# Performance work log

Measured on AMD Instinct MI355X. Metric: run time of the kernel, lower is better.

## Reference

```python
import jax, jax.numpy as jnp
import numpy as np


def conv(x, w, b=None, pad=0):
    y = jax.lax.conv_general_dilated(x, w, (1, 1), [(pad, pad), (pad, pad)],
                                     dimension_numbers=('NCHW', 'OIHW', 'NCHW'))
    if b is not None:
        y = y + b[None, :, None, None]
    return y


def bn(x, g, b, m, v, eps=1e-5):
    scale = g / jnp.sqrt(v + eps)
    return (x - m[None, :, None, None]) * scale[None, :, None, None] + b[None, :, None, None]


def channel_gate(x, w1, b1, w2, b2):
    # avg pool -> MLP -> sigmoid, returns [B, C, 1, 1]
    p = x.mean(axis=(2, 3))                       # [B, C]
    h = jax.nn.relu(p @ w1.T + b1)                # [B, C//r]
    a = h @ w2.T + b2                             # [B, C]
    return jax.nn.sigmoid(a)[:, :, None, None]


def setup_inputs() -> dict:
    key = jax.random.key(0)
    ks = iter(jax.random.split(key, 48))
    B, Cin, H, W = 2, 256, 64, 64
    Ci = Cin // 2          # inter_channels = 128
    Cr = Ci // 16          # gate bottleneck = 8
    def nrm(shape, s=0.05):
        return jax.random.normal(next(ks), shape, jnp.float32) * s
    d = {}
    d['q'] = jax.random.normal(next(ks), (B, Cin, H, W), jnp.float32)
    d['s'] = jax.random.normal(next(ks), (B, Cin, H, W), jnp.float32)
    # Trans_s: conv3x3 + BN
    d['ts_w'] = nrm((Ci, Cin, 3, 3)); d['ts_b'] = jnp.zeros(Ci)
    d['ts_g'] = jnp.ones(Ci); d['ts_be'] = jnp.zeros(Ci)
    d['ts_m'] = nrm((Ci,), 0.01); d['ts_v'] = jnp.ones(Ci)
    # Trans_q: conv3x3 + BN
    d['tq_w'] = nrm((Ci, Cin, 3, 3)); d['tq_b'] = jnp.zeros(Ci)
    d['tq_g'] = jnp.ones(Ci); d['tq_be'] = jnp.zeros(Ci)
    d['tq_m'] = nrm((Ci,), 0.01); d['tq_v'] = jnp.ones(Ci)
    # common_v 1x1
    d['cv_w'] = nrm((Ci, Ci, 1, 1)); d['cv_b'] = jnp.zeros(Ci)
    # key/query 1x1 projections (out = Ci//2)
    d['k1_w'] = nrm((Ci // 2, Ci, 1, 1)); d['k1_b'] = jnp.zeros(Ci // 2)
    d['q1_w'] = nrm((Ci // 2, Ci, 1, 1)); d['q1_b'] = jnp.zeros(Ci // 2)
    d['k2_w'] = nrm((Ci // 2, Ci, 1, 1)); d['k2_b'] = jnp.zeros(Ci // 2)
    d['q2_w'] = nrm((Ci // 2, Ci, 1, 1)); d['q2_b'] = jnp.zeros(Ci // 2)
    # ChannelGate MLP
    d['g1_w'] = nrm((Cr, Ci)); d['g1_b'] = jnp.zeros(Cr)
    d['g2_w'] = nrm((Ci, Cr)); d['g2_b'] = jnp.zeros(Ci)
    # conv_cat: conv3x3 (no bias) + BN
    d['cc_w'] = nrm((Ci, 2 * Ci, 3, 3))
    d['cc_g'] = jnp.ones(Ci); d['cc_be'] = jnp.zeros(Ci)
    d['cc_m'] = nrm((Ci,), 0.01); d['cc_v'] = jnp.ones(Ci)
    return d


def reference(q, s, ts_w, ts_b, ts_g, ts_be, ts_m, ts_v,
              tq_w, tq_b, tq_g, tq_be, tq_m, tq_v,
              cv_w, cv_b, k1_w, k1_b, q1_w, q1_b, k2_w, k2_b, q2_w, q2_b,
              g1_w, g1_b, g2_w, g2_b, cc_w, cc_g, cc_be, cc_m, cc_v):
    # stems: conv3x3 + BN + ReLU
    s = jax.nn.relu(bn(conv(s, ts_w, ts_b, pad=1), ts_g, ts_be, ts_m, ts_v))
    q = jax.nn.relu(bn(conv(q, tq_w, tq_b, pad=1), tq_g, tq_be, tq_m, tq_v))
    B, C, H, W = q.shape
    N = H * W
    # values
    v_q1 = conv(q, cv_w, cv_b)                          # [B,C,H,W]
    v_s1 = conv(s, cv_w, cv_b)
    v_q = v_q1.reshape(B, C, N).transpose(0, 2, 1)      # [B,N,C]
    v_s = v_s1.reshape(B, C, N).transpose(0, 2, 1)
    # dual keys / queries with negation trick
    k1 = conv(s, k1_w, k1_b).reshape(B, C // 2, N)
    k2 = conv(q, k2_w, k2_b).reshape(B, C // 2, N)
    key_cat = jnp.concatenate([k1, -k2], axis=1).transpose(0, 2, 1)   # [B,N,C]
    q1x = conv(s, q1_w, q1_b).reshape(B, C // 2, N)
    q2x = conv(q, q2_w, q2_b).reshape(B, C // 2, N)
    query_cat = jnp.concatenate([q1x, q2x], axis=1)                    # [B,C,N]
    # abs-score attention, dual softmax from the same score matrix
    A_s = jnp.abs(jnp.einsum('bnc,bcm->bnm', key_cat, query_cat))      # [B,N,N]
    att_s = jax.nn.softmax(A_s, axis=-1)
    att_q = jax.nn.softmax(A_s.transpose(0, 2, 1), axis=-1)
    # attend + channel-gate SE fusion + residual
    p_s = jnp.einsum('bnm,bmc->bnc', att_s, v_s).transpose(0, 2, 1).reshape(B, C, H, W)
    E_s = channel_gate(v_s1, g1_w, g1_b, g2_w, g2_b) * p_s + s
    q_s = jnp.einsum('bnm,bmc->bnc', att_q, v_q).transpose(0, 2, 1).reshape(B, C, H, W)
    E_q = channel_gate(v_q1, g1_w, g1_b, g2_w, g2_b) * q_s + q
    # concat + conv3x3(no bias) + BN + ReLU
    cpam = jax.nn.relu(bn(conv(jnp.concatenate([E_q, E_s], axis=1), cc_w, None, pad=1),
                          cc_g, cc_be, cc_m, cc_v))
    return (cpam, E_q, E_s)
```

## Files before the change

### kernel.cpp

```cpp
#include <hip/hip_runtime.h>

typedef __bf16 bf16;
typedef __bf16 v8bf __attribute__((ext_vector_type(8)));
typedef __bf16 v4bf __attribute__((ext_vector_type(4)));
typedef float v4f __attribute__((ext_vector_type(4)));

#define MFMA16(a, b, c) __builtin_amdgcn_mfma_f32_16x16x32_bf16(a, b, c, 0, 0, 0)

__device__ __forceinline__ float sf(float x) {
  if (!(x == x)) return 0.f;
  return fminf(fmaxf(x, -1e30f), 1e30f);
}

__global__ __launch_bounds__(256) void fill_kernel(float* __restrict__ out, float v, int n) {
  int i = blockIdx.x * 256 + threadIdx.x;
  if (i < n) out[i] = v;
}

__global__ __launch_bounds__(256) void prep_kernel(
    const float* __restrict__ ts_w, const float* __restrict__ tq_w,
    const float* ts_b, const float* ts_g, const float* ts_be, const float* ts_m, const float* ts_v,
    const float* tq_b, const float* tq_g, const float* tq_be, const float* tq_m, const float* tq_v,
    bf16* __restrict__ Wt01, float* __restrict__ ss01)
{
  int idx = blockIdx.x * 256 + threadIdx.x;
  if (idx < 589824) {
    int which = idx / 294912;
    int rem = idx - which * 294912;
    int co = rem / 2304;
    int r2 = rem - co * 2304;
    int tap = r2 >> 8;
    int ci = r2 & 255;
    const float* W = which ? tq_w : ts_w;
    Wt01[idx] = (bf16)W[(co * 256 + ci) * 9 + tap];
  } else if (idx < 590080) {
    int i = idx - 589824;
    int which = i >> 7, c = i & 127;
    float g, be, m, vv, bias;
    if (which == 0) { g=ts_g[c]; be=ts_be[c]; m=ts_m[c]; vv=ts_v[c]; bias=ts_b[c]; }
    else            { g=tq_g[c]; be=tq_be[c]; m=tq_m[c]; vv=tq_v[c]; bias=tq_b[c]; }
    float scale = g / sqrtf(vv + 1e-5f);
    ss01[which * 256 + c] = sf(scale);
    ss01[which * 256 + 128 + c] = sf((bias - m) * scale + be);
  }
}

__global__ __launch_bounds__(256) void prep2_kernel(
    const float* __restrict__ cc_w, const float* cc_g, const float* cc_be,
    const float* cc_m, const float* cc_v,
    bf16* __restrict__ Wt2, float* __restrict__ ss_cc)
{
  int idx = blockIdx.x * 256 + threadIdx.x;
  if (idx < 294912) {
    int co = idx / 2304;
    int r2 = idx - co * 2304;
    int tap = r2 >> 8;
    int ci = r2 & 255;
    Wt2[idx] = (bf16)cc_w[(co * 256 + ci) * 9 + tap];
  } else if (idx < 295040) {
    int c = idx - 294912;
    float scale = cc_g[c] / sqrtf(cc_v[c] + 1e-5f);
    ss_cc[c] = sf(scale);
    ss_cc[128 + c] = sf(-cc_m[c] * scale + cc_be[c]);
  }
}

__global__ __launch_bounds__(256) void tr_kernel(
    const float* __restrict__ s_in, const float* __restrict__ q_in, bf16* __restrict__ xin)
{
  int nb = blockIdx.x;
  int z = blockIdx.y;
  const float* in = ((z >> 1) ? q_in : s_in) + (long)(z & 1) * 1048576;
  bf16* out = xin + (long)z * 1048576;
  int t = threadIdx.x, lane = t & 63, w = t >> 6;
  long n = (long)nb * 64 + lane;
#pragma unroll
  for (int i = 0; i < 8; ++i) {
    int c8 = w * 8 + i;
    v8bf o;
#pragma unroll
    for (int j = 0; j < 8; ++j) o[j] = (bf16)in[(long)(c8 * 8 + j) * 4096 + n];
    *(v8bf*)(out + n * 256 + c8 * 8) = o;
  }
}

__global__ __launch_bounds__(256) void convN_kernel(
    const bf16* __restrict__ inA,
    const bf16* __restrict__ Wb, const float* __restrict__ ssb,
    void* __restrict__ out_, int mode)
{
  __shared__ bf16 As[66][40];
  __shared__ bf16 Bs[3][64][40];

  int y = blockIdx.x;
  int co0 = blockIdx.y * 64;
  int z = blockIdx.z;
  int tsr = z >> 1, b = z & 1;

  const bf16 *in0, *in1;
  const bf16* W;
  const float* sp;
  if (mode == 0) {
    in0 = inA + (long)z * 1048576;
    in1 = nullptr;
    W = Wb + (long)tsr * 294912;
    sp = ssb + tsr * 256;
  } else {
    in0 = inA + (long)(2 + b) * 524288;
    in1 = inA + (long)b * 524288;
    W = Wb; sp = ssb;
  }

  int t = threadIdx.x, lane = t & 63, w = t >> 6;
  int l15 = lane & 15, l4 = lane >> 4;
  int wr = (w & 1) * 32, wc = (w >> 1) * 32;
  int ax = t >> 2, ac0 = (t & 3) * 8;
  int bco = t >> 2, bk = (t & 3) * 8;

  v4f acc[2][2] = {};

  auto loadA = [&](int it, v8bf& areg) {
    int dy = it >> 3, ks = it & 7;
    int ysrc = y + dy - 1;
    if ((unsigned)ysrc < 64u) {
      long n = (long)ysrc * 64 + ax;
      int cg = ks * 32 + ac0;
      const bf16* src;
      if (mode == 0)     src = in0 + n * 256 + cg;
      else if (cg < 128) src = in0 + n * 128 + cg;
      else               src = in1 + n * 128 + (cg - 128);
      areg = *(const v8bf*)src;
    } else {
#pragma unroll
      for (int i = 0; i < 8; ++i) areg[i] = (bf16)0.f;
    }
  };
  auto loadB = [&](int it, v8bf* breg) {
    int dy = it >> 3, ks = it & 7;
    const bf16* wk = W + (long)(co0 + bco) * 2304 + dy * 3 * 256 + ks * 32 + bk;
#pragma unroll
    for (int d = 0; d < 3; ++d) breg[d] = *(const v8bf*)(wk + d * 256);
  };

  if (t < 32) As[0][t] = (bf16)0.f;
  else if (t < 64) As[65][t - 32] = (bf16)0.f;

  v8bf areg, breg[3];
  loadA(0, areg);
  loadB(0, breg);

  for (int it = 0; it < 24; ++it) {
    __syncthreads();
    *(v8bf*)&As[ax + 1][ac0] = areg;
#pragma unroll
    for (int d = 0; d < 3; ++d) *(v8bf*)&Bs[d][bco][bk] = breg[d];
    __syncthreads();
    if (it < 23) { loadA(it + 1, areg); loadB(it + 1, breg); }
#pragma unroll
    for (int d = 0; d < 3; ++d) {
      v8bf af0 = *(const v8bf*)&As[wr + d + l15][l4 * 8];
      v8bf af1 = *(const v8bf*)&As[wr + 16 + d + l15][l4 * 8];
#pragma unroll
      for (int j = 0; j < 2; ++j) {
        v8bf bfr = *(const v8bf*)&Bs[d][wc + j * 16 + l15][l4 * 8];
        acc[0][j] = MFMA16(af0, bfr, acc[0][j]);
        acc[1][j] = MFMA16(af1, bfr, acc[1][j]);
      }
    }
  }
#pragma unroll
  for (int i = 0; i < 2; ++i) {
    int nb = y * 64 + wr + i * 16 + l4 * 4;
#pragma unroll
    for (int j = 0; j < 2; ++j) {
      int c = co0 + wc + j * 16 + l15;
      float scale = sp[c], shift = sp[128 + c];
      if (mode == 0) {
        bf16* o = (bf16*)out_ + ((long)(tsr * 2 + b) * 4096 + nb) * 128 + c;
#pragma unroll
        for (int r = 0; r < 4; ++r)
          o[r * 128] = (bf16)sf(fmaxf(acc[i][j][r] * scale + shift, 0.f));
      } else {
        v4f pk;
#pragma unroll
        for (int r = 0; r < 4; ++r)
          pk[r] = sf(fmaxf(acc[i][j][r] * scale + shift, 0.f));
        *(v4f*)((float*)out_ + ((long)b * 128 + c) * 4096 + nb) = pk;
      }
    }
  }
}

__global__ __launch_bounds__(256) void conv1_kernel(
    const bf16* __restrict__ feat_base,
    const float* __restrict__ cv_w, const float* __restrict__ k1_w, const float* __restrict__ q1_w,
    const float* __restrict__ k2_w, const float* __restrict__ q2_w,
    const float* __restrict__ cv_b, const float* __restrict__ k1_b, const float* __restrict__ q1_b,
    const float* __restrict__ k2_b, const float* __restrict__ q2_b,
    bf16* __restrict__ v_base, bf16* __restrict__ keyT, bf16* __restrict__ queryT,
    float* __restrict__ pmean)
{
  int nt = blockIdx.x;
  int br = blockIdx.z >> 1, b = blockIdx.z & 1;
  long zid = br * 2 + b;
  const bf16* feat = feat_base + zid * 524288 + (long)nt * 4096;

  __shared__ bf16 As[32][40];
  __shared__ bf16 Bs[256][40];

  int t = threadIdx.x, lane = t & 63, w = t >> 6;
  int l15 = lane & 15, l4 = lane >> 4;
  int wr = (w & 1) * 16, wc = (w >> 1) * 128;

  const float* wrow;
  bool negk = false;
  if (t < 128)       wrow = cv_w + (long)t * 128;
  else if (t < 192) { wrow = (br ? k2_w : k1_w) + (long)(t - 128) * 128; negk = (br != 0); }
  else               wrow = (br ? q2_w : q1_w) + (long)(t - 192) * 128;

  v4f acc[8] = {};
  int ap = t >> 2, ak = (t & 3) * 8;

  for (int ks = 0; ks < 4; ++ks) {
    int ci0 = ks * 32;
    v8bf av;
    if (t < 128) av = *(const v8bf*)(feat + ap * 128 + ci0 + ak);
    float wv[32];
#pragma unroll
    for (int u = 0; u < 32; ++u) wv[u] = wrow[ci0 + u];
    if (negk) {
#pragma unroll
      for (int u = 0; u < 32; ++u) wv[u] = -wv[u];
    }
    __syncthreads();
    if (t < 128) *(v8bf*)&As[ap][ak] = av;
#pragma unroll
    for (int u = 0; u < 32; ++u) Bs[t][u] = (bf16)wv[u];
    __syncthreads();
    v8bf af = *(const v8bf*)&As[wr + l15][l4 * 8];
#pragma unroll
    for (int j = 0; j < 8; ++j) {
      v8bf bfr = *(const v8bf*)&Bs[wc + j * 16 + l15][l4 * 8];
      acc[j] = MFMA16(af, bfr, acc[j]);
    }
  }

  int nb = nt * 32 + wr + l4 * 4;
#pragma unroll
  for (int j = 0; j < 8; ++j) {
    int c = wc + j * 16 + l15;
    float bv;
    if (c < 128)      bv = cv_b[c];
    else if (c < 192) bv = br ? -k2_b[c - 128] : k1_b[c - 128];
    else              bv = (br ? q2_b : q1_b)[c - 192];
    float v0 = sf(acc[j][0] + bv), v1 = sf(acc[j][1] + bv);
    float v2 = sf(acc[j][2] + bv), v3 = sf(acc[j][3] + bv);
    if (c < 128) {
      long off = (long)(nb >> 5) * 4096 + (c >> 4) * 512 + ((nb >> 3) & 3) * 128 +
                 (c & 15) * 8 + (nb & 7);
      v4bf pk;
      pk[0] = (bf16)v0; pk[1] = (bf16)v1; pk[2] = (bf16)v2; pk[3] = (bf16)v3;
      *(v4bf*)(v_base + zid * 524288 + off) = pk;
      float s = v0 + v1 + v2 + v3;
      s += __shfl_xor(s, 16, 64);
      s += __shfl_xor(s, 32, 64);
      if (l4 == 0) atomicAdd(&pmean[zid * 128 + c], s);
    } else if (c < 192) {
      int cc = (c - 128) + br * 64;
      long off = (long)(nb >> 4) * 2048 + (cc >> 5) * 512 + ((cc >> 3) & 3) * 128 +
                 (nb & 15) * 8 + (cc & 7);
      bf16* kp = keyT + (long)b * 524288 + off;
      kp[0] = (bf16)v0; kp[8] = (bf16)v1; kp[16] = (bf16)v2; kp[24] = (bf16)v3;
    } else {
      int cc = (c - 192) + br * 64;
      long off = (long)(nb >> 4) * 2048 + (cc >> 5) * 512 + ((cc >> 3) & 3) * 128 +
                 (nb & 15) * 8 + (cc & 7);
      bf16* qp = queryT + (long)b * 524288 + off;
      qp[0] = (bf16)v0; qp[8] = (bf16)v1; qp[16] = (bf16)v2; qp[24] = (bf16)v3;
    }
  }
}

__global__ __launch_bounds__(128) void gate2_kernel(
    const float* __restrict__ pmean, const float* __restrict__ g1_w, const float* __restrict__ g1_b,
    const float* __restrict__ g2_w, const float* __restrict__ g2_b, float* __restrict__ gate)
{
  __shared__ float p[128];
  __shared__ float h[8];
  int z = blockIdx.x, t = threadIdx.x;
  p[t] = pmean[z * 128 + t] * (1.f / 4096.f);
  __syncthreads();
  if (t < 8) {
    float a = g1_b[t];
    for (int c = 0; c < 128; ++c) a += g1_w[t * 128 + c] * p[c];
    h[t] = fmaxf(a, 0.f);
  }
  __syncthreads();
  float a = g2_b[t];
#pragma unroll
  for (int j = 0; j < 8; ++j) a += g2_w[t * 8 + j] * h[j];
  gate[z * 128 + t] = sf(1.f / (1.f + __expf(-a)));
}

__global__ __launch_bounds__(256, 2) void apply_kernel(
    const bf16* __restrict__ keyT, const bf16* __restrict__ queryT,
    const bf16* __restrict__ v_base, const float* __restrict__ gate,
    bf16* __restrict__ feat_base, float* __restrict__ d_out)
{
  int nt = blockIdx.x, br = blockIdx.z >> 1, b = blockIdx.z & 1;
  int n0 = nt * 32;
  const bf16* Xf = (br ? queryT : keyT) + (long)b * 524288 + (long)(n0 >> 4) * 2048;
  const bf16* Yf = (br ? keyT : queryT) + (long)b * 524288;
  const bf16* Vf = v_base + (long)(br * 2 + b) * 524288;
  const float* gt = gate + (br * 2 + b) * 128;
  bf16* feat = feat_base + (long)(br * 2 + b) * 524288 + (long)n0 * 128;

  __shared__ bf16 Ps[2][32][72];
  __shared__ float rps[4][32];

  int t = threadIdx.x, lane = t & 63, w = t >> 6;
  int l15 = lane & 15, l4 = lane >> 4;
  int wm = w * 16;
  int wr = (w & 1) * 16;
  int wc = (w >> 1) * 64;

  v8bf af[2][4];
#pragma unroll
  for (int i = 0; i < 2; ++i)
#pragma unroll
    for (int k = 0; k < 4; ++k)
      af[i][k] = *(const v8bf*)(Xf + i * 2048 + k * 512 + lane * 8);

  v4f acc[4] = {};
  float rp[2][4] = {};

  auto loadBy = [&](int m0, v8bf* by) {
    const bf16* p = Yf + (long)((m0 >> 4) + w) * 2048 + lane * 8;
#pragma unroll
    for (int k = 0; k < 4; ++k) by[k] = *(const v8bf*)(p + k * 512);
  };
  auto loadVb = [&](int m0, v8bf* vb) {
    const bf16* p = Vf + (long)(m0 >> 5) * 4096 + ((w >> 1) * 4) * 512 + lane * 8;
#pragma unroll
    for (int j = 0; j < 4; ++j)
#pragma unroll
      for (int k = 0; k < 2; ++k)
        vb[j * 2 + k] = *(const v8bf*)(p + k * 4096 + j * 512);
  };

  v8bf byA[4], byB[4], vbA[8], vbB[8];
  loadBy(0, byA);
  loadVb(0, vbA);

  auto subiter = [&](v8bf (&by)[4], v8bf (&vb)[8], v8bf (&byN)[4], v8bf (&vbN)[8],
                     int psb, int m0n, bool pf) {
    v4f sacc[2] = {};
#pragma unroll
    for (int k = 0; k < 4; ++k)
#pragma unroll
      for (int i = 0; i < 2; ++i)
        sacc[i] = MFMA16(af[i][k], by[k], sacc[i]);
    if (pf) { loadBy(m0n, byN); loadVb(m0n, vbN); }
#pragma unroll
    for (int i = 0; i < 2; ++i)
#pragma unroll
      for (int r = 0; r < 4; ++r) {
        float e = __expf(fminf(fabsf(sacc[i][r]), 80.f) - 50.f);
        rp[i][r] += e;
        Ps[psb][i * 16 + l4 * 4 + r][wm + l15] = (bf16)e;
      }
    asm volatile("s_waitcnt lgkmcnt(0)" ::: "memory");
    __builtin_amdgcn_s_barrier();
#pragma unroll
    for (int k = 0; k < 2; ++k) {
      v8bf p0 = *(const v8bf*)&Ps[psb][wr + l15][k * 32 + l4 * 8];
#pragma unroll
      for (int j = 0; j < 4; ++j)
        acc[j] = MFMA16(p0, vb[j * 2 + k], acc[j]);
    }
  };

  for (int mt2 = 0; mt2 < 32; ++mt2) {
    int mA = mt2 * 128;
    subiter(byA, vbA, byB, vbB, 0, mA + 64, true);
    subiter(byB, vbB, byA, vbA, 1, mA + 128, mt2 < 31);
  }

#pragma unroll
  for (int i = 0; i < 2; ++i)
#pragma unroll
    for (int r = 0; r < 4; ++r) {
      float v = rp[i][r];
      v += __shfl_xor(v, 1, 64);
      v += __shfl_xor(v, 2, 64);
      v += __shfl_xor(v, 4, 64);
      v += __shfl_xor(v, 8, 64);
      if (l15 == 0) rps[w][i * 16 + l4 * 4 + r] = v;
    }
  __syncthreads();

  float* outE = d_out + (long)(br ? 1 : 2) * 1048576 + (long)b * 524288;
  int rowt = wr + l4 * 4;
  float dv[4];
#pragma unroll
  for (int r = 0; r < 4; ++r)
    dv[r] = fmaxf(rps[0][rowt + r] + rps[1][rowt + r] + rps[2][rowt + r] + rps[3][rowt + r],
                  1e-30f);
#pragma unroll
  for (int j = 0; j < 4; ++j) {
    int c = wc + j * 16 + l15;
    float g = gt[c];
    v4f pk;
#pragma unroll
    for (int r = 0; r < 4; ++r) {
      long fi = (long)(rowt + r) * 128 + c;
      float fv = (float)feat[fi];
      float val = sf(acc[j][r] / dv[r] * g + fv);
      pk[r] = val;
      feat[fi] = (bf16)val;
    }
    *(v4f*)(outE + (long)c * 4096 + n0 + rowt) = pk;
  }
}

extern "C" void kernel_launch(void* const* d_in, const int* in_sizes, int n_in,
                              void* d_out, int out_size, void* d_ws, size_t ws_size,
                              hipStream_t stream)
{
  if (n_in != 33 || in_sizes[0] != 2097152 || in_sizes[2] != 294912 ||
      in_sizes[14] != 16384 || out_size != 3145728) {
    fill_kernel<<<12288, 256, 0, stream>>>((float*)d_out, 100.0f, 3145728);
    return;
  }
  if (ws_size < 12582912) {
    fill_kernel<<<12288, 256, 0, stream>>>((float*)d_out, 1.0f, 3145728);
    return;
  }

  const float* q_in = (const float*)d_in[0];
  const float* s_in = (const float*)d_in[1];
  char* ob = (char*)d_out;
  float* outf = (float*)d_out;

  float* gate  = (float*)(ob + 0);
  float* pmean = (float*)(ob + 2048);
  bf16*  xin   = (bf16*)(ob + 4194304);

  char* ws = (char*)d_ws;
  bf16*  sfeat  = (bf16*)(ws + 0);
  bf16*  vs     = (bf16*)(ws + 4194304);
  bf16*  keyT   = (bf16*)(ws + 8388608);
  bf16*  queryT = (bf16*)(ws + 10485760);
  bf16*  Wt01   = (bf16*)(ws + 8388608);
  float* ss01   = (float*)(ws + 10485760);
  bf16*  Wt2    = (bf16*)(ws + 8388608);
  float* ss_cc  = (float*)(ws + 8978432);

  prep_kernel<<<2306, 256, 0, stream>>>(
      (const float*)d_in[2], (const float*)d_in[8],
      (const float*)d_in[3], (const float*)d_in[4], (const float*)d_in[5],
      (const float*)d_in[6], (const float*)d_in[7],
      (const float*)d_in[9], (const float*)d_in[10], (const float*)d_in[11],
      (const float*)d_in[12], (const float*)d_in[13],
      Wt01, ss01);

  fill_kernel<<<2, 256, 0, stream>>>(pmean, 0.0f, 512);

  tr_kernel<<<dim3(64, 4), 256, 0, stream>>>(s_in, q_in, xin);

  convN_kernel<<<dim3(64, 2, 4), 256, 0, stream>>>(xin, Wt01, ss01, sfeat, 0);

  conv1_kernel<<<dim3(128, 1, 4), 256, 0, stream>>>(
      sfeat,
      (const float*)d_in[14], (const float*)d_in[16], (const float*)d_in[18],
      (const float*)d_in[20], (const float*)d_in[22],
      (const float*)d_in[15], (const float*)d_in[17], (const float*)d_in[19],
      (const float*)d_in[21], (const float*)d_in[23],
      vs, keyT, queryT, pmean);

  gate2_kernel<<<4, 128, 0, stream>>>(pmean, (const float*)d_in[24], (const float*)d_in[25],
                                      (const float*)d_in[26], (const float*)d_in[27], gate);

  apply_kernel<<<dim3(128, 1, 4), 256, 0, stream>>>(keyT, queryT, vs, gate, sfeat, outf);

  prep2_kernel<<<1153, 256, 0, stream>>>(
      (const float*)d_in[28], (const float*)d_in[29], (const float*)d_in[30],
      (const float*)d_in[31], (const float*)d_in[32], Wt2, ss_cc);

  convN_kernel<<<dim3(64, 2, 2), 256, 0, stream>>>(sfeat, Wt2, ss_cc, outf, 1);
}
```

Baseline: 266.1 us.

## Split attention key dimension across two blocks with atomic partial sums and combine pass

The attention apply kernel now splits the 4096-long key/value sweep into two halves via blockIdx.y, doubling the grid from 512 to 1024 blocks. Each half atomically adds its unnormalized numerator into the output buffer and its softmax row sums into a new dvsum buffer. A new combine kernel then normalizes, applies the channel gate, adds the residual feature, and writes both the bf16 feature and the fp32 output. Occupancy hint is raised to 4 blocks per CU. The aim is better load across CUs, at the cost of float atomics, an extra zero-fill of 8 MB, and an extra pass. The split-softmax merge is valid because both halves use the same fixed exponent offset.

```diff
diff --git a/kernel.cpp b/kernel.cpp
--- a/kernel.cpp
+++ b/kernel.cpp
@@ -302,18 +302,17 @@
   gate[z * 128 + t] = sf(1.f / (1.f + __expf(-a)));
 }
 
-__global__ __launch_bounds__(256, 2) void apply_kernel(
+__global__ __launch_bounds__(256, 4) void apply_kernel(
     const bf16* __restrict__ keyT, const bf16* __restrict__ queryT,
-    const bf16* __restrict__ v_base, const float* __restrict__ gate,
-    bf16* __restrict__ feat_base, float* __restrict__ d_out)
-{
-  int nt = blockIdx.x, br = blockIdx.z >> 1, b = blockIdx.z & 1;
+    const bf16* __restrict__ v_base,
+    float* __restrict__ d_out, float* __restrict__ dvsum)
+{
+  int nt = blockIdx.x, ms = blockIdx.y, br = blockIdx.z >> 1, b = blockIdx.z & 1;
   int n0 = nt * 32;
+  int mbase = ms * 2048;
   const bf16* Xf = (br ? queryT : keyT) + (long)b * 524288 + (long)(n0 >> 4) * 2048;
   const bf16* Yf = (br ? keyT : queryT) + (long)b * 524288;
   const bf16* Vf = v_base + (long)(br * 2 + b) * 524288;
-  const float* gt = gate + (br * 2 + b) * 128;
-  bf16* feat = feat_base + (long)(br * 2 + b) * 524288 + (long)n0 * 128;
 
   __shared__ bf16 Ps[2][32][72];
   __shared__ float rps[4][32];
@@ -349,8 +348,8 @@
   };
 
   v8bf byA[4], byB[4], vbA[8], vbB[8];
-  loadBy(0, byA);
-  loadVb(0, vbA);
+  loadBy(mbase, byA);
+  loadVb(mbase, vbA);
 
   auto subiter = [&](v8bf (&by)[4], v8bf (&vb)[8], v8bf (&byN)[4], v8bf (&vbN)[8],
                      int psb, int m0n, bool pf) {
@@ -380,10 +379,10 @@
     }
   };
 
-  for (int mt2 = 0; mt2 < 32; ++mt2) {
-    int mA = mt2 * 128;
+  for (int mt2 = 0; mt2 < 16; ++mt2) {
+    int mA = mbase + mt2 * 128;
     subiter(byA, vbA, byB, vbB, 0, mA + 64, true);
-    subiter(byB, vbB, byA, vbA, 1, mA + 128, mt2 < 31);
+    subiter(byB, vbB, byA, vbA, 1, mA + 128, mt2 < 15);
   }
 
 #pragma unroll
@@ -399,28 +398,68 @@
     }
   __syncthreads();
 
-  float* outE = d_out + (long)(br ? 1 : 2) * 1048576 + (long)b * 524288;
+  if (t < 32) {
+    float s = rps[0][t] + rps[1][t] + rps[2][t] + rps[3][t];
+    atomicAdd(&dvsum[(long)(br * 2 + b) * 4096 + n0 + t], s);
+  }
+
+  float* num = d_out + (long)(br ? 1 : 2) * 1048576 + (long)b * 524288;
   int rowt = wr + l4 * 4;
-  float dv[4];
-#pragma unroll
-  for (int r = 0; r < 4; ++r)
-    dv[r] = fmaxf(rps[0][rowt + r] + rps[1][rowt + r] + rps[2][rowt + r] + rps[3][rowt + r],
-                  1e-30f);
 #pragma unroll
   for (int j = 0; j < 4; ++j) {
     int c = wc + j * 16 + l15;
-    float g = gt[c];
-    v4f pk;
-#pragma unroll
-    for (int r = 0; r < 4; ++r) {
-      long fi = (long)(rowt + r) * 128 + c;
-      float fv = (float)feat[fi];
-      float val = sf(acc[j][r] / dv[r] * g + fv);
-      pk[r] = val;
-      feat[fi] = (bf16)val;
-    }
-    *(v4f*)(outE + (long)c * 4096 + n0 + rowt) = pk;
-  }
+    float* np = num + (long)c * 4096 + n0 + rowt;
+#pragma unroll
+    for (int r = 0; r < 4; ++r) atomicAdd(np + r, acc[j][r]);
+  }
+}
+
+__global__ __launch_bounds__(256) void combine_kernel(
+    float* __restrict__ d_out, const float* __restrict__ dvsum, const float* __restrict__ gate,
+    bf16* __restrict__ feat_base)
+{
+  int nt = blockIdx.x;
+  int z = blockIdx.y;
+  int br = z >> 1, b = z & 1;
+  int n0 = nt * 32;
+  float* outE = d_out + (long)(br ? 1 : 2) * 1048576 + (long)b * 524288;
+  bf16* feat = feat_base + (long)z * 524288 + (long)n0 * 128;
+  const float* gt = gate + z * 128;
+  const float* dvp = dvsum + (long)z * 4096 + n0;
+
+  __shared__ float Ln[128][33];
+  __shared__ float dvl[32];
+
+  int t = threadIdx.x;
+  int n = t & 31, cb = (t >> 5) * 16;
+#pragma unroll
+  for (int i = 0; i < 16; ++i) Ln[cb + i][n] = outE[(long)(cb + i) * 4096 + n0 + n];
+  if (t < 32) dvl[t] = fmaxf(dvp[t], 1e-30f);
+  __syncthreads();
+
+  int nn = t >> 3, cc = (t & 7) * 16;
+  float dv = dvl[nn];
+  v8bf f0 = *(const v8bf*)(feat + (long)nn * 128 + cc);
+  v8bf f1 = *(const v8bf*)(feat + (long)nn * 128 + cc + 8);
+  v8bf o0, o1;
+#pragma unroll
+  for (int i = 0; i < 8; ++i) {
+    float val = sf(Ln[cc + i][nn] / dv * gt[cc + i] + (float)f0[i]);
+    Ln[cc + i][nn] = val;
+    o0[i] = (bf16)val;
+  }
+#pragma unroll
+  for (int i = 0; i < 8; ++i) {
+    float val = sf(Ln[cc + 8 + i][nn] / dv * gt[cc + 8 + i] + (float)f1[i]);
+    Ln[cc + 8 + i][nn] = val;
+    o1[i] = (bf16)val;
+  }
+  *(v8bf*)(feat + (long)nn * 128 + cc) = o0;
+  *(v8bf*)(feat + (long)nn * 128 + cc + 8) = o1;
+  __syncthreads();
+
+#pragma unroll
+  for (int i = 0; i < 16; ++i) outE[(long)(cb + i) * 4096 + n0 + n] = Ln[cb + i][n];
 }
 
 extern "C" void kernel_launch(void* const* d_in, const int* in_sizes, int n_in,
@@ -444,6 +483,7 @@
 
   float* gate  = (float*)(ob + 0);
   float* pmean = (float*)(ob + 2048);
+  float* dvsum = (float*)(ob + 4096);
   bf16*  xin   = (bf16*)(ob + 4194304);
 
   char* ws = (char*)d_ws;
@@ -464,11 +504,13 @@
       (const float*)d_in[12], (const float*)d_in[13],
       Wt01, ss01);
 
-  fill_kernel<<<2, 256, 0, stream>>>(pmean, 0.0f, 512);
+  fill_kernel<<<66, 256, 0, stream>>>(pmean, 0.0f, 16896);
 
   tr_kernel<<<dim3(64, 4), 256, 0, stream>>>(s_in, q_in, xin);
 
   convN_kernel<<<dim3(64, 2, 4), 256, 0, stream>>>(xin, Wt01, ss01, sfeat, 0);
+
+  fill_kernel<<<8192, 256, 0, stream>>>((float*)(ob + 4194304), 0.0f, 2097152);
 
   conv1_kernel<<<dim3(128, 1, 4), 256, 0, stream>>>(
       sfeat,
@@ -481,7 +523,9 @@
   gate2_kernel<<<4, 128, 0, stream>>>(pmean, (const float*)d_in[24], (const float*)d_in[25],
                                       (const float*)d_in[26], (const float*)d_in[27], gate);
 
-  apply_kernel<<<dim3(128, 1, 4), 256, 0, stream>>>(keyT, queryT, vs, gate, sfeat, outf);
+  apply_kernel<<<dim3(128, 2, 4), 256, 0, stream>>>(keyT, queryT, vs, outf, dvsum);
+
+  combine_kernel<<<dim3(128, 4), 256, 0, stream>>>(outf, dvsum, gate, sfeat);
 
   prep2_kernel<<<1153, 256, 0, stream>>>(
       (const float*)d_in[28], (const float*)d_in[29], (const float*)d_in[30],
```

Result: slower. 454.5 us (+70.8%).
